# Performance work log

Measured on AMD Instinct MI355X. Metric: run time of the kernel, lower is better.

Reference implementation:

```python
import jax, jax.numpy as jnp
from jax import lax
import numpy as np

M, CLS, K, DL, DC, DO, BD = 87, 65, 128, 128, 128, 2048, 256
B, H, W = 256, 7, 7


def _c1(x, Wt, b):
    # 1x1 Conv2d: [B,Cin,H,W] -> [B,Cout,H,W]
    return jnp.einsum('oc,bchw->bohw', Wt, x) + b[None, :, None, None]


def _pagerank(edge, v_init, p=0.85, iters=100):
    # torch: transition = adj / adj.sum(dim=1)  (broadcast divides COLUMNS by row-sums)
    n = edge.shape[0]
    Wpr = p * edge / jnp.sum(edge, axis=1)[None, :]
    s = v_init * n                                  # [B,n,1]
    coef = (1.0 - p) / n
    def body(i, xv):
        zx = coef * jnp.sum(xv, axis=1, keepdims=True)      # z_T @ x -> [B,1,1]
        return jnp.einsum('ij,bjo->bio', Wpr, xv) + s * zx
    xv = lax.fori_loop(0, iters, body, s)
    nrm = jnp.sqrt(jnp.sum(xv * xv, axis=1, keepdims=True))  # F.normalize(dim=1)
    xv = xv / jnp.maximum(nrm, 1e-12)
    return (v_init + xv).reshape(v_init.shape[0], -1)        # [B,n]


def setup_inputs() -> dict:
    key = jax.random.key(0)
    ks = jax.random.split(key, 24)
    def w(k, shape, s=0.02):
        return jax.random.normal(k, shape, jnp.float32) * s
    rng = np.random.default_rng(0)
    A = (rng.random((M, M)) < 0.08).astype(np.float32)
    A = np.maximum(A, A.T)
    np.fill_diagonal(A, 1.0)   # symmetric adjacency with self-loops (degrees > 0)
    return {
        'x': jax.random.normal(ks[0], (B, DO, H, W), jnp.float32),
        'Wb': w(ks[1], (BD, DO)), 'bb': w(ks[2], (BD,), 0.01),
        'Wfc': w(ks[3], (CLS, BD)), 'Wfc2': w(ks[4], (CLS, BD)),
        'Wo1': w(ks[5], (4 * DL, DO)), 'bo1': w(ks[6], (4 * DL,), 0.01),
        'Wo2': w(ks[7], (DL, 4 * DL)), 'bo2': w(ks[8], (DL,), 0.01),
        'Wa': w(ks[9], (M, DL)), 'ba': w(ks[10], (M,), 0.01),
        'Wps': w(ks[11], (DC, DL)), 'bps': w(ks[12], (DC,), 0.01),
        'node_p': jax.random.uniform(ks[13], (K, M), jnp.float32, -0.1, 0.1),
        'Wg': w(ks[14], (DC, DC + K)), 'bg': w(ks[15], (DC,), 0.01),
        'Wsp': w(ks[16], (DL, DC)), 'bsp': w(ks[17], (DL,), 0.01),
        'Ws': w(ks[18], (1, DC + DL)), 'bs': w(ks[19], (1,), 0.01),
        'Wox1': w(ks[20], (4 * DL, DL)), 'box1': w(ks[21], (4 * DL,), 0.01),
        'Wox2': w(ks[22], (DO, 4 * DL)), 'box2': w(ks[23], (DO,), 0.01),
        'edge': jnp.asarray(A),
    }


def reference(x, Wb, bb, Wfc, Wfc2, Wo1, bo1, Wo2, bo2, Wa, ba, Wps, bps,
              node_p, Wg, bg, Wsp, bsp, Ws, bs, Wox1, box1, Wox2, box2, edge):
    Bsz, _, hl, wl = x.shape
    HW = hl * wl

    # global pooled branch
    x_p = jnp.mean(x, axis=(2, 3))                           # [B,2048]
    features_p = x_p @ Wb.T + bb                             # [B,256]
    pre_output = features_p @ Wfc.T                          # [B,65]
    pre_score = jax.nn.softmax(lax.stop_gradient(pre_output), axis=1)

    # personalized pagerank over the semantic graph (constant wrt grads)
    v_init = jnp.concatenate(
        [jnp.zeros((Bsz, M - CLS), x.dtype), pre_score], axis=1)[:, :, None]
    v_y = lax.stop_gradient(_pagerank(edge, v_init))         # [B,87]

    # local feature reduction 2048 -> 512 -> 128
    x_l = _c1(_c1(x, Wo1, bo1), Wo2, bo2)                    # [B,128,7,7]

    a = _c1(x_l, Wa, ba).reshape(Bsz, M, HW).transpose(0, 2, 1)   # [B,HW,87]
    ps = _c1(x_l, Wps, bps).reshape(Bsz, DC, HW)                  # [B,128,HW]
    m1 = jax.nn.relu(jnp.matmul(ps, a))                           # [B,128,87]

    # replicate torch's exact (k, B*m) reshape + flat v_y broadcast
    node = jnp.broadcast_to(node_p[None], (Bsz, K, M)).reshape(K, Bsz * M)
    node = (v_y.reshape(-1) * node).reshape(Bsz, K, M)

    g = jnp.einsum('oc,bcm->bom', Wg, jnp.concatenate([node, m1], axis=1)) \
        + bg[None, :, None]                                   # [B,128,87]

    # D^-1/2 A D^-1/2 graph propagation
    Dinv = jnp.sum(edge, axis=0) ** -0.5
    edge_norm = Dinv[:, None] * edge * Dinv[None, :]
    m2 = jax.nn.relu(jnp.einsum('bcm,mn->bcn', g, edge_norm))  # [B,128,87]

    sp = jnp.einsum('oc,bcm->bom', Wsp, m2) + bsp[None, :, None]  # [B,128,87]

    # conv_s over concat(m2_expand, x_expand) is separable: avoid the
    # [B,256,HW,87] tensor entirely (1 output channel, 1x1 kernel).
    Ws1, Ws2 = Ws[0, :DC], Ws[0, DC:]
    t_node = jnp.einsum('c,bcm->bm', Ws1, m2)                  # [B,87]
    t_pix = jnp.einsum('c,bcp->bp', Ws2, x_l.reshape(Bsz, DL, HW))  # [B,HW]
    s_logits = t_node[:, :, None] + t_pix[:, None, :] + bs[0]  # [B,87,HW]
    s_att = jax.nn.softmax(s_logits, axis=1)                   # softmax over nodes

    m3 = jax.nn.relu(jnp.matmul(sp, s_att)).reshape(Bsz, DL, hl, wl)
    m3 = _c1(_c1(m3, Wox1, box1), Wox2, box2)                  # [B,2048,7,7]

    feature_aug = jnp.mean(m3, axis=(2, 3)) @ Wb.T + bb
    features = features_p + feature_aug
    outputs2 = features @ Wfc2.T
    softmax_outputs = jax.nn.softmax(outputs2, axis=1)
    return (features, outputs2, softmax_outputs, pre_output, features_p)
```

## Files before the change

kernel.cpp:

```cpp
#include <hip/hip_runtime.h>
#include <cmath>


typedef __attribute__((ext_vector_type(8))) short short8;
typedef __attribute__((ext_vector_type(4))) short s16x4;
typedef __attribute__((ext_vector_type(4))) float f32x4;

constexpr size_t OFF_W12BF = 0;
constexpr size_t OFF_T1BF  = 131072;
constexpr size_t OFF_WBBF  = 262144;
constexpr size_t OFF_XPBF  = 524288;
constexpr size_t OFF_WAPBF = 786432;
constexpr size_t OFF_WG2BF = 800768;
constexpr size_t OFF_ENPBF = 808960;
constexpr size_t OFF_B215  = 813568;
constexpr size_t OFF_B12   = 813792;
constexpr size_t OFF_WPR   = 813920;
constexpr size_t OFF_BTMP  = 821496;
constexpr size_t OFF_WC    = 823544;
constexpr size_t OFF_BC    = 856312;
constexpr size_t OFF_VY    = 856568;
constexpr size_t OFF_NT    = 878848;
constexpr size_t OFF_PART  = 901376;

__device__ __forceinline__ unsigned short f2bf(float f) {
  unsigned u = __builtin_bit_cast(unsigned, f);
  u += 0x7fffu + ((u >> 16) & 1u);
  return (unsigned short)(u >> 16);
}
__device__ __forceinline__ float bf2f(unsigned short s) {
  return __builtin_bit_cast(float, ((unsigned)s) << 16);
}

__global__ __launch_bounds__(256) void ksetup_all(
    const float* __restrict__ Wb,  const float* __restrict__ bb,
    const float* __restrict__ Wa,  const float* __restrict__ ba,
    const float* __restrict__ Wps, const float* __restrict__ bps,
    const float* __restrict__ Wg,  const float* __restrict__ edge,
    const float* __restrict__ Wo2, const float* __restrict__ Wo1,
    const float* __restrict__ Wox2,const float* __restrict__ Wox1,
    const float* __restrict__ box1,const float* __restrict__ box2,
    const float* __restrict__ bo1, const float* __restrict__ bo2,
    float* __restrict__ ws, float* __restrict__ featp)
{
  __shared__ alignas(16) short As[64*72];
  __shared__ alignas(16) short Bs[64*72];
  int blk = blockIdx.x, tid = threadIdx.x;
  if (blk < 2048) {
    int idx = blk*256 + tid;
    ((unsigned short*)(ws+OFF_WBBF))[idx] = f2bf(Wb[idx]);
  } else if (blk < 2304) {
    int idx = (blk-2048)*256 + tid;
    featp[idx] = bb[idx & 255];
  } else if (blk < 2432) {
    int idx = (blk-2304)*256 + tid;
    ws[OFF_WC + idx] = 0.f;
  } else if (blk < 2544) {
    int idx = (blk-2432)*256 + tid;
    int r = idx >> 7, c = idx & 127;
    float v;
    if (r < 128)      v = Wps[r*128 + c];
    else if (r < 215) v = Wa[(r-128)*128 + c];
    else              v = 0.f;
    ((unsigned short*)(ws+OFF_WAPBF))[idx] = f2bf(v);
  } else if (blk < 2608) {
    int idx = (blk-2544)*256 + tid;
    int o = idx >> 7, d = idx & 127;
    ((unsigned short*)(ws+OFF_WG2BF))[idx] = f2bf(Wg[o*256 + 128 + d]);
  } else if (blk < 2644) {
    int idx = (blk-2608)*256 + tid;
    int m = idx / 96, n = idx % 96;
    float v = 0.f;
    if (m < 87 && n < 87) {
      float sm = 0.f, sn = 0.f;
      for (int k = 0; k < 87; ++k) { sm += edge[k*87+m]; sn += edge[k*87+n]; }
      v = edge[m*87+n] / sqrtf(sm*sn);
    }
    ((unsigned short*)(ws+OFF_ENPBF))[idx] = f2bf(v);
  } else if (blk < 2674) {
    int idx = (blk-2644)*256 + tid;
    if (idx < 87*87) {
      int j = idx % 87;
      float rs = 0.f;
      for (int k = 0; k < 87; ++k) rs += edge[j*87+k];
// ... 84 lines not shown
  const float* xb = x + ((size_t)b*2048 + q*512)*49;

  int p4A = tid % 13, cA = tid / 13;
  int tB = tid + 512;
  int p4B = tB % 13, cB = tB / 13;
  bool hasB = (tid < 320);

  float fA[4], fB[4];
  {
    if (p4A < 12) {
      float4 v = *(const float4*)(xb + cA*49 + p4A*4);
      fA[0]=v.x; fA[1]=v.y; fA[2]=v.z; fA[3]=v.w;
    } else fA[0] = xb[cA*49 + 48];
    if (hasB) {
      if (p4B < 12) {
        float4 v = *(const float4*)(xb + cB*49 + p4B*4);
        fB[0]=v.x; fB[1]=v.y; fB[2]=v.z; fB[3]=v.w;
      } else fB[0] = xb[cB*49 + 48];
    }
  }

  f32x4 acc[4];
  #pragma unroll
  for (int i = 0; i < 4; ++i) acc[i] = (f32x4)(0.f);

  for (int kci = 0; kci < 8; ++kci) {
    short* bt = Bt[kci & 1];
    if (p4A < 12) {
      #pragma unroll
      for (int i = 0; i < 4; ++i) bt[(p4A*4+i)*72 + cA] = (short)f2bf(fA[i]);
    } else bt[48*72 + cA] = (short)f2bf(fA[0]);
    if (hasB) {
      if (p4B < 12) {
        #pragma unroll
        for (int i = 0; i < 4; ++i) bt[(p4B*4+i)*72 + cB] = (short)f2bf(fB[i]);
      } else bt[48*72 + cB] = (short)f2bf(fB[0]);
    }
    __syncthreads();
    if (kci < 7) {
      const float* xc = xb + (size_t)(kci+1)*64*49;
      if (p4A < 12) {
        float4 v = *(const float4*)(xc + cA*49 + p4A*4);
        fA[0]=v.x; fA[1]=v.y; fA[2]=v.z; fA[3]=v.w;
      } else fA[0] = xc[cA*49 + 48];
      if (hasB) {
        if (p4B < 12) {
          float4 v = *(const float4*)(xc + cB*49 + p4B*4);
          fB[0]=v.x; fB[1]=v.y; fB[2]=v.z; fB[3]=v.w;
        } else fB[0] = xc[cB*49 + 48];
      }
    }
    const short* wr = w12bf + (size_t)(w*16 + lane16)*2048 + q*512 + kci*64 + quad*8;
    short8 a0 = *(const short8*)(wr);
    short8 a1 = *(const short8*)(wr + 32);
    #pragma unroll
    for (int ni = 0; ni < 4; ++ni) {
      const short* br = bt + (ni*16 + lane16)*72 + quad*8;
      short8 b0 = *(const short8*)(br);
      short8 b1 = *(const short8*)(br + 32);
      acc[ni] = __builtin_amdgcn_mfma_f32_16x16x32_bf16(a0, b0, acc[ni], 0, 0, 0);
      acc[ni] = __builtin_amdgcn_mfma_f32_16x16x32_bf16(a1, b1, acc[ni], 0, 0, 0);
    }
    if (tid < 64) {
      float s = 0.f;
      for (int p = 0; p < 49; ++p)
        s += bf2f((unsigned short)bt[p*72 + tid]);
      xpbf[(size_t)b*2048 + q*512 + kci*64 + tid] = (short)f2bf(s * (1.f/49.f));
    }
  }
  float* po = part + ((size_t)q*256 + b)*6656;
  #pragma unroll
  for (int ni = 0; ni < 4; ++ni) {
    int p = ni*16 + lane16;
    if (p < 49) {
      #pragma unroll
      for (int r = 0; r < 4; ++r) {
        int o = w*16 + quad*4 + r;
        po[o*52 + p] = acc[ni][r];
      }
    }
  }
}

__global__ __launch_bounds__(256) void kwcf(const float* __restrict__ Wb,
                                            const float* __restrict__ bb,
                                            const short* __restrict__ xpbf,
                                            float* __restrict__ featp,
                                            float* __restrict__ ws)
{
  __shared__ alignas(16) short As[64*72];
  __shared__ alignas(16) short Bs[64*72];
  int blk = blockIdx.x, tid = threadIdx.x;
  if (blk < 64) {
    const short* wbbf = (const short*)(ws+OFF_WBBF);
    const short* t1s  = (const short*)(ws+OFF_T1BF);
    int i0 = (blk & 3)*64, j0 = ((blk >> 2) & 1)*64, kc0 = (blk >> 3)*256;
    int w = tid >> 6, l = tid & 63, quad = l >> 4, lane16 = l & 15;
    f32x4 acc[4];
    #pragma unroll
    for (int i = 0; i < 4; ++i) acc[i] = (f32x4)(0.f);
    for (int kc = kc0; kc < kc0+256; kc += 64) {
      for (int t = tid; t < 512; t += 256) {
        int r = t >> 3, c8 = t & 7;
        *(short8*)&As[r*72 + c8*8] = *(const short8*)&wbbf[(size_t)(i0+r)*2048 + kc + c8*8];
      }
      for (int t = tid; t < 1024; t += 256) {
        int kr = t >> 4, n4 = t & 15;
        s16x4 v = *(const s16x4*)&t1s[(size_t)(kc+kr)*128 + j0 + n4*4];
        Bs[(n4*4+0)*72 + kr] = v[0];
        Bs[(n4*4+1)*72 + kr] = v[1];
        Bs[(n4*4+2)*72 + kr] = v[2];
        Bs[(n4*4+3)*72 + kr] = v[3];
      }
      __syncthreads();
      #pragma unroll
      for (int ks = 0; ks < 2; ++ks) {
        short8 a = *(const short8*)&As[(w*16+lane16)*72 + ks*32 + quad*8];
        #pragma unroll
        for (int nt = 0; nt < 4; ++nt) {
          short8 b8 = *(const short8*)&Bs[(nt*16+lane16)*72 + ks*32 + quad*8];
          acc[nt] = __builtin_amdgcn_mfma_f32_16x16x32_bf16(a, b8, acc[nt], 0, 0, 0);
        }
      }
      __syncthreads();
    }
    #pragma unroll
    for (int nt = 0; nt < 4; ++nt)
      #pragma unroll
      for (int r = 0; r < 4; ++r)
        atomicAdd(&ws[OFF_WC + (size_t)(i0 + w*16 + quad*4 + r)*128 + j0 + nt*16 + lane16], acc[nt][r]);
  } else if (blk < 128) {
    int j = (blk-64)*4 + (tid >> 6), l = tid & 63;
    float s = 0.f;
    for (int c = l; c < 2048; c += 64) s += Wb[(size_t)j*2048 + c] * ws[OFF_BTMP + c];
    for (int off = 32; off; off >>= 1) s += __shfl_down(s, off, 64);
    if (l == 0) ws[OFF_BC + j] = s + bb[j];
  } else {
    const short* wbbf = (const short*)(ws+OFF_WBBF);
    int idx = blk - 128;
    int i0 = (idx & 3)*64, j0 = ((idx >> 2) & 3)*64, kc0 = (idx >> 4)*256;
    int w = tid >> 6, l = tid & 63, quad = l >> 4, lane16 = l & 15;
    f32x4 acc[4];
    #pragma unroll
    for (int i = 0; i < 4; ++i) acc[i] = (f32x4)(0.f);
    for (int kc = kc0; kc < kc0+256; kc += 32) {
      short8 a = *(const short8*)&xpbf[(size_t)(i0 + w*16 + lane16)*2048 + kc + quad*8];
      #pragma unroll
      for (int nt = 0; nt < 4; ++nt) {
        short8 b8 = *(const short8*)&wbbf[(size_t)(j0 + nt*16 + lane16)*2048 + kc + quad*8];
        acc[nt] = __builtin_amdgcn_mfma_f32_16x16x32_bf16(a, b8, acc[nt], 0, 0, 0);
      }
    }
    #pragma unroll
    for (int nt = 0; nt < 4; ++nt)
      #pragma unroll
      for (int r = 0; r < 4; ++r)
        atomicAdd(&featp[(size_t)(i0 + w*16 + quad*4 + r)*256 + j0 + nt*16 + lane16], acc[nt][r]);
  }
}

__global__ __launch_bounds__(128, 1) void kpr(const float* __restrict__ featp,
                                              const float* __restrict__ Wfc,
                                              const float* __restrict__ wpr,
                                              float* __restrict__ preo,
                                              float* __restrict__ vy)
{
  __shared__ alignas(16) float fpr[256];
  __shared__ alignas(16) float po[68];
  __shared__ alignas(16) float vs[2][88];
  __shared__ float red[2];
  int b = blockIdx.x, tid = threadIdx.x;
  fpr[tid] = featp[b*256 + tid];
  fpr[tid+128] = featp[b*256 + 128 + tid];
  __syncthreads();
  if (tid < 65) {
    float s = 0.f;
    for (int c = 0; c < 256; c += 4) {
      float4 w4 = *(const float4*)&Wfc[tid*256 + c];
      s += w4.x*fpr[c] + w4.y*fpr[c+1] + w4.z*fpr[c+2] + w4.w*fpr[c+3];
    }
    po[tid] = s;
    preo[b*65 + tid] = s;
  }
  __syncthreads();
  if (tid < 64) {
    float v = po[tid];
    if (tid == 0) v = fmaxf(v, po[64]);
    float mx = v;
    #pragma unroll
    for (int off = 32; off; off >>= 1) mx = fmaxf(mx, __shfl_down(mx, off, 64));
    mx = __shfl(mx, 0, 64);
    float e = expf(po[tid]-mx) + ((tid == 0) ? expf(po[64]-mx) : 0.f);
    float sm = e;
    #pragma unroll
    for (int off = 32; off; off >>= 1) sm += __shfl_down(sm, off, 64);
    if (tid == 0) { red[0] = mx; red[1] = 1.f/sm; }
  }
  __syncthreads();
  float vinit = 0.f;
  if (tid >= 22 && tid < 87) vinit = expf(po[tid-22]-red[0]) * red[1];
  float s_i = vinit * 87.f;
  float wrow[87];
  if (tid < 87) {
    float add = s_i * (0.15f/87.0f);
    #pragma unroll
    for (int j = 0; j < 87; ++j) wrow[j] = wpr[tid*87 + j] + add;
    vs[0][tid] = s_i;
  }
  __syncthreads();
  for (int it = 0; it < 64; ++it) {
    const float* vc = vs[it & 1];
    if (tid < 87) {
      float nv = 0.f;
      #pragma unroll
      for (int j4 = 0; j4 < 21; ++j4) {
        float4 v4 = *(const float4*)&vc[j4*4];
        nv += wrow[j4*4+0]*v4.x + wrow[j4*4+1]*v4.y + wrow[j4*4+2]*v4.z + wrow[j4*4+3]*v4.w;
      }
      nv += wrow[84]*vc[84] + wrow[85]*vc[85] + wrow[86]*vc[86];
      vs[(it+1) & 1][tid] = nv;
    }
    __syncthreads();
  }
  if (tid < 64) {
    float v = vs[0][tid]*vs[0][tid];
    if (tid < 23) v += vs[0][64+tid]*vs[0][64+tid];
    #pragma unroll
    for (int off = 32; off; off >>= 1) v += __shfl_down(v, off, 64);
    if (tid == 0) red[0] = 1.f / fmaxf(sqrtf(v), 1e-12f);
  }
  __syncthreads();
  if (tid < 87) vy[b*87 + tid] = vinit + vs[0][tid]*red[0];
}

__global__ __launch_bounds__(256) void knode(const float* __restrict__ Wg,
                                             const float* __restrict__ node_p,
                                             const float* __restrict__ vy,
                                             float* __restrict__ nt)
{
  int idx = blockIdx.x*256 + threadIdx.x;
  int par = idx / 11264;
  int r = idx % 11264;
  int o = r / 88, m = r % 88;
  float v = 0.f;
  if (m < 87) {
    float s = 0.f;
    for (int k = 0; k < 128; ++k)
      s += Wg[o*256+k] * node_p[k*87+m] * vy[(par*128+k)*87+m];
    v = s;
  }
  nt[idx] = v;
}

__global__ __launch_bounds__(512) void kgraph_all(
    const float* __restrict__ part,  const float* __restrict__ b12,
    const short* __restrict__ wapbf, const float* __restrict__ b215,
    const short* __restrict__ wg2bf, const float* __restrict__ nt,
    const float* __restrict__ bg,    const short* __restrict__ enpbf,
    const float* __restrict__ Wsp,   const float* __restrict__ bsp,
    const float* __restrict__ Ws,    const float* __restrict__ wc,
    const float* __restrict__ bc,    const float* __restrict__ featp,
    const float* __restrict__ Wfc2,
    float* __restrict__ feat, float* __restrict__ out2, float* __restrict__ soft)
{
  extern __shared__ char smraw[];
  short* XT = (short*)smraw;
  short* At = XT + 8704;
  short* M1 = At + 16128;
  short* G  = M1 + 13056;
  short* M2 = G  + 13312;
  float* fb  = (float*)(M2 + 13312);
  float* wsm = fb;
  float* tnb = fb + 96;
  float* zs  = fb + 192;
  float* m3s = fb + 320;
  float* fs  = fb + 448;
  float* o2s = fb + 704;
  float* red = fb + 776;

  int b = blockIdx.x, tid = threadIdx.x;
  int w = tid >> 6, l = tid & 63, quad = l >> 4, lane16 = l & 15;

  const float* p0 = part + (size_t)b*6656;
  const float* p1 = p0 + (size_t)256*6656;
  const float* p2 = p1 + (size_t)256*6656;
  const float* p3 = p2 + (size_t)256*6656;
  for (int t = tid; t < 6656; t += 512) {
    int o = t / 52, p = t % 52;
    XT[p*136 + o] = (short)f2bf(p0[t] + p1[t] + p2[t] + p3[t] + b12[o]);
  }
  for (int t = tid; t < 1536; t += 512) {
    int p = 52 + t/128, o = t % 128;
    XT[p*136 + o] = 0;
  }
  __syncthreads();

  for (int t = w; t < 56; t += 8) {
    int mt = t >> 2, n4 = t & 3;
    f32x4 acc = (f32x4)(0.f);
    #pragma unroll
    for (int ks = 0; ks < 4; ++ks) {
      short8 a  = *(const short8*)&wapbf[(size_t)(mt*16+lane16)*128 + ks*32 + quad*8];
      short8 b8 = *(const short8*)&XT[(n4*16+lane16)*136 + ks*32 + quad*8];
      acc = __builtin_amdgcn_mfma_f32_16x16x32_bf16(a, b8, acc, 0, 0, 0);
    }
    int p = n4*16 + lane16;
    #pragma unroll
    for (int r = 0; r < 4; ++r) {
      int rr = mt*16 + quad*4 + r;
      At[rr*72 + p] = (p < 49) ? (short)f2bf(acc[r] + b215[rr]) : (short)0;
    }
  }
  __syncthreads();

  for (int t = w; t < 48; t += 8) {
    int mt = t / 8, n4 = t % 8;
    f32x4 acc = (f32x4)(0.f);
    #pragma unroll
    for (int ks = 0; ks < 2; ++ks) {
      short8 a  = *(const short8*)&At[(128 + mt*16 + lane16)*72 + ks*32 + quad*8];
      short8 b8 = *(const short8*)&At[(n4*16+lane16)*72 + ks*32 + quad*8];
      acc = __builtin_amdgcn_mfma_f32_16x16x32_bf16(a, b8, acc, 0, 0, 0);
    }
    int d = n4*16 + lane16;
    #pragma unroll
    for (int r = 0; r < 4; ++r) {
      int m = mt*16 + quad*4 + r;
      M1[m*136 + d] = (short)f2bf(fmaxf(acc[r], 0.f));
    }
  }
  __syncthreads();

  const float* ntb = nt + (size_t)(b & 1)*11264;
  for (int t = w; t < 48; t += 8) {
    int mt = t / 6, n4 = t % 6;
    f32x4 acc = (f32x4)(0.f);
    #pragma unroll
    for (int ks = 0; ks < 4; ++ks) {
      short8 a  = *(const short8*)&wg2bf[(size_t)(mt*16+lane16)*128 + ks*32 + quad*8];
      short8 b8 = *(const short8*)&M1[(n4*16+lane16)*136 + ks*32 + quad*8];
      acc = __builtin_amdgcn_mfma_f32_16x16x32_bf16(a, b8, acc, 0, 0, 0);
    }
    int m = n4*16 + lane16;
    #pragma unroll
    for (int r = 0; r < 4; ++r) {
      int o = mt*16 + quad*4 + r;
      float v = acc[r] + bg[o] + ((m < 88) ? ntb[o*88 + m] : 0.f);
      G[o*104 + m] = (short)f2bf(v);
    }
  }
  __syncthreads();

  for (int t = w; t < 48; t += 8) {
    int mt = t / 6, n4 = t % 6;
    f32x4 acc = (f32x4)(0.f);
    #pragma unroll
    for (int ks = 0; ks < 3; ++ks) {
      short8 a  = *(const short8*)&G[(mt*16+lane16)*104 + ks*32 + quad*8];
      short8 b8 = *(const short8*)&enpbf[(size_t)(n4*16+lane16)*96 + ks*32 + quad*8];
      acc = __builtin_amdgcn_mfma_f32_16x16x32_bf16(a, b8, acc, 0, 0, 0);
    }
    int n = n4*16 + lane16;
    #pragma unroll
    for (int r = 0; r < 4; ++r) {
      int c = mt*16 + quad*4 + r;
      M2[c*104 + n] = (short)f2bf(fmaxf(acc[r], 0.f));
    }
  }
  __syncthreads();

  if (tid < 87) {
    float s = 0.f;
    for (int c = 0; c < 128; ++c) s += Ws[c] * bf2f((unsigned short)M2[c*104 + tid]);
    tnb[tid] = s;
  }
  __syncthreads();
  if (tid < 64) {
    float v = tnb[tid];
    if (tid < 23) v = fmaxf(v, tnb[64+tid]);
    float mx = v;
    #pragma unroll
    for (int off = 32; off; off >>= 1) mx = fmaxf(mx, __shfl_down(mx, off, 64));
    mx = __shfl(mx, 0, 64);
    float e0 = expf(tnb[tid]-mx);
    float e1 = (tid < 23) ? expf(tnb[64+tid]-mx) : 0.f;
    float sm = e0 + e1;
    #pragma unroll
    for (int off = 32; off; off >>= 1) sm += __shfl_down(sm, off, 64);
    sm = __shfl(sm, 0, 64);
    float inv = 1.f/sm;
    wsm[tid] = e0*inv;
    if (tid < 23) wsm[64+tid] = e1*inv;
  }
  __syncthreads();
  if (tid < 128) {
    float s = 0.f;
    for (int m = 0; m < 87; ++m) s += bf2f((unsigned short)M2[tid*104 + m]) * wsm[m];
    zs[tid] = s;
  }
  __syncthreads();
  if (tid < 128) {
    float s = 0.f;
    for (int c = 0; c < 128; ++c) s += Wsp[tid*128 + c] * zs[c];
    m3s[tid] = fmaxf(s + bsp[tid], 0.f);
  }
  __syncthreads();

  if (tid < 256) {
    float s = 0.f;
    #pragma unroll 4
    for (int d4 = 0; d4 < 32; ++d4) {
      float4 w4 = *(const float4*)&wc[tid*128 + d4*4];
      s += w4.x*m3s[d4*4] + w4.y*m3s[d4*4+1] + w4.z*m3s[d4*4+2] + w4.w*m3s[d4*4+3];
    }
    float f = featp[b*256 + tid] + bc[tid] + s;
    fs[tid] = f;
    feat[b*256 + tid] = f;
  }
  __syncthreads();
  if (tid < 65) {
    float s = 0.f;
    for (int j = 0; j < 256; ++j) s += Wfc2[tid*256 + j] * fs[j];
    out2[b*65 + tid] = s;
    o2s[tid] = s;
  }
  __syncthreads();
  if (tid < 64) {
    float v = o2s[tid];
    if (tid == 0) v = fmaxf(v, o2s[64]);
    float mx = v;
    #pragma unroll
    for (int off = 32; off; off >>= 1) mx = fmaxf(mx, __shfl_down(mx, off, 64));
    mx = __shfl(mx, 0, 64);
    float e = expf(o2s[tid]-mx) + ((tid == 0) ? expf(o2s[64]-mx) : 0.f);
    float sm = e;
    #pragma unroll
    for (int off = 32; off; off >>= 1) sm += __shfl_down(sm, off, 64);
    if (tid == 0) { red[0] = mx; red[1] = 1.f/sm; }
  }
  __syncthreads();
  if (tid < 65) soft[b*65 + tid] = expf(o2s[tid]-red[0]) * red[1];
}

extern "C" void kernel_launch(void* const* d_in, const int* in_sizes, int n_in,
                              void* d_out, int out_size, void* d_ws, size_t ws_size,
                              hipStream_t stream)
{
  (void)in_sizes; (void)n_in; (void)out_size; (void)ws_size;
  const float* x      = (const float*)d_in[0];
  const float* Wb     = (const float*)d_in[1];
  const float* bb     = (const float*)d_in[2];
  const float* Wfc    = (const float*)d_in[3];
  const float* Wfc2   = (const float*)d_in[4];
  const float* Wo1    = (const float*)d_in[5];
  const float* bo1    = (const float*)d_in[6];
  const float* Wo2    = (const float*)d_in[7];
  const float* bo2    = (const float*)d_in[8];
  const float* Wa     = (const float*)d_in[9];
  const float* ba     = (const float*)d_in[10];
  const float* Wps    = (const float*)d_in[11];
  const float* bps    = (const float*)d_in[12];
  const float* node_p = (const float*)d_in[13];
  const float* Wg     = (const float*)d_in[14];
  const float* bg     = (const float*)d_in[15];
  const float* Wsp    = (const float*)d_in[16];
  const float* bsp    = (const float*)d_in[17];
  const float* Ws     = (const float*)d_in[18];
  const float* Wox1   = (const float*)d_in[20];
  const float* box1   = (const float*)d_in[21];
  const float* Wox2   = (const float*)d_in[22];
  const float* box2   = (const float*)d_in[23];
  const float* edge   = (const float*)d_in[24];

  float* ws   = (float*)d_ws;
  float* out  = (float*)d_out;
  float* feat  = out;
  float* out2  = out + 65536;
  float* soft  = out + 82176;
  float* preo  = out + 98816;
  float* featp = out + 115456;

  ksetup_all<<<3347, 256, 0, stream>>>(Wb, bb, Wa, ba, Wps, bps, Wg, edge,
                                       Wo2, Wo1, Wox2, Wox1, box1, box2, bo1, bo2,
                                       ws, featp);
  kmain5<<<dim3(256,4), 512, 0, stream>>>(x, (const short*)(ws + OFF_W12BF),
                                          (short*)(ws + OFF_XPBF), ws + OFF_PART);
  kwcf<<<256, 256, 0, stream>>>(Wb, bb, (const short*)(ws + OFF_XPBF), featp, ws);
  kpr<<<256, 128, 0, stream>>>(featp, Wfc, ws + OFF_WPR, preo, ws + OFF_VY);
  knode<<<88, 256, 0, stream>>>(Wg, node_p, ws + OFF_VY, ws + OFF_NT);
  kgraph_all<<<256, 512, 132144, stream>>>(ws + OFF_PART, ws + OFF_B12,
                                           (const short*)(ws + OFF_WAPBF),
                                           ws + OFF_B215,
                                           (const short*)(ws + OFF_WG2BF),
                                           ws + OFF_NT, bg,
                                           (const short*)(ws + OFF_ENPBF),
                                           Wsp, bsp, Ws,
                                           ws + OFF_WC, ws + OFF_BC, featp, Wfc2,
                                           feat, out2, soft);
}
```

Before: 363.0 us.

## Merge tail kernels into one cooperative kernel with grid syncs

Replaces the four tail launches (kwcf, kpr, knode, kgraph_all) with a single cooperative kernel of 256 blocks x 512 threads that separates the phases with grid.sync(). The goal is to cut launch and inter-kernel gap overhead. Several small per-block loops (Wfc GEMV, the PageRank matvec, the node contraction, the Ws/Wsp/Wfc2 reductions) now split work four ways across lanes and combine with shuffles. The cost is that a 132 KB LDS allocation limits occupancy to one block per CU, so all 256 blocks must be co-resident, and the grid barriers add their own latency.

```diff
diff --git a/kernel.cpp b/kernel.cpp
--- a/kernel.cpp
+++ b/kernel.cpp
@@ -1,5 +1,8 @@
 #include <hip/hip_runtime.h>
+#include <hip/hip_cooperative_groups.h>
 #include <cmath>
+
+namespace cg = cooperative_groups;
 
 
 typedef __attribute__((ext_vector_type(8))) short short8;
@@ -250,364 +253,402 @@
   }
 }
 
-__global__ __launch_bounds__(256) void kwcf(const float* __restrict__ Wb,
-                                            const float* __restrict__ bb,
-                                            const short* __restrict__ xpbf,
-                                            float* __restrict__ featp,
-                                            float* __restrict__ ws)
-{
-  __shared__ alignas(16) short As[64*72];
-  __shared__ alignas(16) short Bs[64*72];
-  int blk = blockIdx.x, tid = threadIdx.x;
-  if (blk < 64) {
-    const short* wbbf = (const short*)(ws+OFF_WBBF);
-    const short* t1s  = (const short*)(ws+OFF_T1BF);
-    int i0 = (blk & 3)*64, j0 = ((blk >> 2) & 1)*64, kc0 = (blk >> 3)*256;
-    int w = tid >> 6, l = tid & 63, quad = l >> 4, lane16 = l & 15;
-    f32x4 acc[4];
-    #pragma unroll
-    for (int i = 0; i < 4; ++i) acc[i] = (f32x4)(0.f);
-    for (int kc = kc0; kc < kc0+256; kc += 64) {
-      for (int t = tid; t < 512; t += 256) {
-        int r = t >> 3, c8 = t & 7;
-        *(short8*)&As[r*72 + c8*8] = *(const short8*)&wbbf[(size_t)(i0+r)*2048 + kc + c8*8];
-      }
-      for (int t = tid; t < 1024; t += 256) {
-        int kr = t >> 4, n4 = t & 15;
-        s16x4 v = *(const s16x4*)&t1s[(size_t)(kc+kr)*128 + j0 + n4*4];
-        Bs[(n4*4+0)*72 + kr] = v[0];
-        Bs[(n4*4+1)*72 + kr] = v[1];
-        Bs[(n4*4+2)*72 + kr] = v[2];
-        Bs[(n4*4+3)*72 + kr] = v[3];
-      }
-      __syncthreads();
-      #pragma unroll
-      for (int ks = 0; ks < 2; ++ks) {
-        short8 a = *(const short8*)&As[(w*16+lane16)*72 + ks*32 + quad*8];
-        #pragma unroll
-        for (int nt = 0; nt < 4; ++nt) {
-          short8 b8 = *(const short8*)&Bs[(nt*16+lane16)*72 + ks*32 + quad*8];
-          acc[nt] = __builtin_amdgcn_mfma_f32_16x16x32_bf16(a, b8, acc[nt], 0, 0, 0);
-        }
-      }
-      __syncthreads();
-    }
-    #pragma unroll
-    for (int nt = 0; nt < 4; ++nt)
-      #pragma unroll
-      for (int r = 0; r < 4; ++r)
-        atomicAdd(&ws[OFF_WC + (size_t)(i0 + w*16 + quad*4 + r)*128 + j0 + nt*16 + lane16], acc[nt][r]);
-  } else if (blk < 128) {
-    int j = (blk-64)*4 + (tid >> 6), l = tid & 63;
-    float s = 0.f;
-    for (int c = l; c < 2048; c += 64) s += Wb[(size_t)j*2048 + c] * ws[OFF_BTMP + c];
-    for (int off = 32; off; off >>= 1) s += __shfl_down(s, off, 64);
-    if (l == 0) ws[OFF_BC + j] = s + bb[j];
-  } else {
-    const short* wbbf = (const short*)(ws+OFF_WBBF);
-    int idx = blk - 128;
-    int i0 = (idx & 3)*64, j0 = ((idx >> 2) & 3)*64, kc0 = (idx >> 4)*256;
-    int w = tid >> 6, l = tid & 63, quad = l >> 4, lane16 = l & 15;
-    f32x4 acc[4];
-    #pragma unroll
-    for (int i = 0; i < 4; ++i) acc[i] = (f32x4)(0.f);
-    for (int kc = kc0; kc < kc0+256; kc += 32) {
-      short8 a = *(const short8*)&xpbf[(size_t)(i0 + w*16 + lane16)*2048 + kc + quad*8];
-      #pragma unroll
-      for (int nt = 0; nt < 4; ++nt) {
-        short8 b8 = *(const short8*)&wbbf[(size_t)(j0 + nt*16 + lane16)*2048 + kc + quad*8];
-        acc[nt] = __builtin_amdgcn_mfma_f32_16x16x32_bf16(a, b8, acc[nt], 0, 0, 0);
-      }
-    }
-    #pragma unroll
-    for (int nt = 0; nt < 4; ++nt)
-      #pragma unroll
-      for (int r = 0; r < 4; ++r)
-        atomicAdd(&featp[(size_t)(i0 + w*16 + quad*4 + r)*256 + j0 + nt*16 + lane16], acc[nt][r]);
-  }
-}
-
-__global__ __launch_bounds__(128, 1) void kpr(const float* __restrict__ featp,
-                                              const float* __restrict__ Wfc,
-                                              const float* __restrict__ wpr,
-                                              float* __restrict__ preo,
-                                              float* __restrict__ vy)
-{
-  __shared__ alignas(16) float fpr[256];
-  __shared__ alignas(16) float po[68];
-  __shared__ alignas(16) float vs[2][88];
-  __shared__ float red[2];
-  int b = blockIdx.x, tid = threadIdx.x;
-  fpr[tid] = featp[b*256 + tid];
-  fpr[tid+128] = featp[b*256 + 128 + tid];
-  __syncthreads();
-  if (tid < 65) {
-    float s = 0.f;
-    for (int c = 0; c < 256; c += 4) {
-      float4 w4 = *(const float4*)&Wfc[tid*256 + c];
-      s += w4.x*fpr[c] + w4.y*fpr[c+1] + w4.z*fpr[c+2] + w4.w*fpr[c+3];
-    }
-    po[tid] = s;
-    preo[b*65 + tid] = s;
-  }
-  __syncthreads();
-  if (tid < 64) {
-    float v = po[tid];
-    if (tid == 0) v = fmaxf(v, po[64]);
-    float mx = v;
-    #pragma unroll
-    for (int off = 32; off; off >>= 1) mx = fmaxf(mx, __shfl_down(mx, off, 64));
-    mx = __shfl(mx, 0, 64);
-    float e = expf(po[tid]-mx) + ((tid == 0) ? expf(po[64]-mx) : 0.f);
-    float sm = e;
-    #pragma unroll
-    for (int off = 32; off; off >>= 1) sm += __shfl_down(sm, off, 64);
-    if (tid == 0) { red[0] = mx; red[1] = 1.f/sm; }
-  }
-  __syncthreads();
-  float vinit = 0.f;
-  if (tid >= 22 && tid < 87) vinit = expf(po[tid-22]-red[0]) * red[1];
-  float s_i = vinit * 87.f;
-  float wrow[87];
-  if (tid < 87) {
-    float add = s_i * (0.15f/87.0f);
-    #pragma unroll
-    for (int j = 0; j < 87; ++j) wrow[j] = wpr[tid*87 + j] + add;
-    vs[0][tid] = s_i;
-  }
-  __syncthreads();
-  for (int it = 0; it < 64; ++it) {
-    const float* vc = vs[it & 1];
-    if (tid < 87) {
-      float nv = 0.f;
-      #pragma unroll
-      for (int j4 = 0; j4 < 21; ++j4) {
-        float4 v4 = *(const float4*)&vc[j4*4];
-        nv += wrow[j4*4+0]*v4.x + wrow[j4*4+1]*v4.y + wrow[j4*4+2]*v4.z + wrow[j4*4+3]*v4.w;
-      }
-      nv += wrow[84]*vc[84] + wrow[85]*vc[85] + wrow[86]*vc[86];
-      vs[(it+1) & 1][tid] = nv;
-    }
-    __syncthreads();
-  }
-  if (tid < 64) {
-    float v = vs[0][tid]*vs[0][tid];
-    if (tid < 23) v += vs[0][64+tid]*vs[0][64+tid];
-    #pragma unroll
-    for (int off = 32; off; off >>= 1) v += __shfl_down(v, off, 64);
-    if (tid == 0) red[0] = 1.f / fmaxf(sqrtf(v), 1e-12f);
-  }
-  __syncthreads();
-  if (tid < 87) vy[b*87 + tid] = vinit + vs[0][tid]*red[0];
-}
-
-__global__ __launch_bounds__(256) void knode(const float* __restrict__ Wg,
-                                             const float* __restrict__ node_p,
-                                             const float* __restrict__ vy,
-                                             float* __restrict__ nt)
-{
-  int idx = blockIdx.x*256 + threadIdx.x;
-  int par = idx / 11264;
-  int r = idx % 11264;
-  int o = r / 88, m = r % 88;
-  float v = 0.f;
-  if (m < 87) {
-    float s = 0.f;
-    for (int k = 0; k < 128; ++k)
-      s += Wg[o*256+k] * node_p[k*87+m] * vy[(par*128+k)*87+m];
-    v = s;
-  }
-  nt[idx] = v;
-}
-
-__global__ __launch_bounds__(512) void kgraph_all(
-    const float* __restrict__ part,  const float* __restrict__ b12,
-    const short* __restrict__ wapbf, const float* __restrict__ b215,
-    const short* __restrict__ wg2bf, const float* __restrict__ nt,
-    const float* __restrict__ bg,    const short* __restrict__ enpbf,
-    const float* __restrict__ Wsp,   const float* __restrict__ bsp,
-    const float* __restrict__ Ws,    const float* __restrict__ wc,
-    const float* __restrict__ bc,    const float* __restrict__ featp,
-    const float* __restrict__ Wfc2,
-    float* __restrict__ feat, float* __restrict__ out2, float* __restrict__ soft)
+__global__ __launch_bounds__(512) void ktail(
+    const float* __restrict__ Wb,  const float* __restrict__ bb,
+    const float* __restrict__ Wfc, const float* __restrict__ Wg,
+    const float* __restrict__ node_p, const float* __restrict__ bg,
+    const float* __restrict__ Wsp, const float* __restrict__ bsp,
+    const float* __restrict__ Ws,  const float* __restrict__ Wfc2,
+    const short* __restrict__ xpbf,
+    float* __restrict__ ws, float* __restrict__ featp,
+    float* __restrict__ preo, float* __restrict__ feat,
+    float* __restrict__ out2, float* __restrict__ soft)
 {
   extern __shared__ char smraw[];
-  short* XT = (short*)smraw;
-  short* At = XT + 8704;
-  short* M1 = At + 16128;
-  short* G  = M1 + 13056;
-  short* M2 = G  + 13312;
-  float* fb  = (float*)(M2 + 13312);
-  float* wsm = fb;
-  float* tnb = fb + 96;
-  float* zs  = fb + 192;
-  float* m3s = fb + 320;
-  float* fs  = fb + 448;
-  float* o2s = fb + 704;
-  float* red = fb + 776;
-
-  int b = blockIdx.x, tid = threadIdx.x;
-  int w = tid >> 6, l = tid & 63, quad = l >> 4, lane16 = l & 15;
-
-  const float* p0 = part + (size_t)b*6656;
-  const float* p1 = p0 + (size_t)256*6656;
-  const float* p2 = p1 + (size_t)256*6656;
-  const float* p3 = p2 + (size_t)256*6656;
-  for (int t = tid; t < 6656; t += 512) {
-    int o = t / 52, p = t % 52;
-    XT[p*136 + o] = (short)f2bf(p0[t] + p1[t] + p2[t] + p3[t] + b12[o]);
+  cg::grid_group grid = cg::this_grid();
+  const int tid = threadIdx.x;
+  const int bx = blockIdx.x;
+
+  {
+    int sub = tid >> 8, stid = tid & 255;
+    int oblk = bx*2 + sub;
+    if (bx < 128) {
+      if (oblk < 64) {
+        short* As = (short*)(smraw + sub*18432);
+        short* Bs = As + 4608;
+        const short* wbbf = (const short*)(ws+OFF_WBBF);
+        const short* t1s  = (const short*)(ws+OFF_T1BF);
+        int i0 = (oblk & 3)*64, j0 = ((oblk >> 2) & 1)*64, kc0 = (oblk >> 3)*256;
+        int w = stid >> 6, l = stid & 63, quad = l >> 4, lane16 = l & 15;
+        f32x4 acc[4];
+        #pragma unroll
+        for (int i = 0; i < 4; ++i) acc[i] = (f32x4)(0.f);
+        for (int kc = kc0; kc < kc0+256; kc += 64) {
+          for (int t = stid; t < 512; t += 256) {
+            int r = t >> 3, c8 = t & 7;
+            *(short8*)&As[r*72 + c8*8] = *(const short8*)&wbbf[(size_t)(i0+r)*2048 + kc + c8*8];
+          }
+          for (int t = stid; t < 1024; t += 256) {
+            int kr = t >> 4, n4 = t & 15;
+            s16x4 v = *(const s16x4*)&t1s[(size_t)(kc+kr)*128 + j0 + n4*4];
+            Bs[(n4*4+0)*72 + kr] = v[0];
+            Bs[(n4*4+1)*72 + kr] = v[1];
+            Bs[(n4*4+2)*72 + kr] = v[2];
+            Bs[(n4*4+3)*72 + kr] = v[3];
+          }
+          __syncthreads();
+          #pragma unroll
+          for (int ks = 0; ks < 2; ++ks) {
+            short8 a = *(const short8*)&As[(w*16+lane16)*72 + ks*32 + quad*8];
+            #pragma unroll
+            for (int nt4 = 0; nt4 < 4; ++nt4) {
+              short8 b8 = *(const short8*)&Bs[(nt4*16+lane16)*72 + ks*32 + quad*8];
+              acc[nt4] = __builtin_amdgcn_mfma_f32_16x16x32_bf16(a, b8, acc[nt4], 0, 0, 0);
+            }
+          }
+          __syncthreads();
+        }
+        #pragma unroll
+        for (int nt4 = 0; nt4 < 4; ++nt4)
+          #pragma unroll
+          for (int r = 0; r < 4; ++r)
+            atomicAdd(&ws[OFF_WC + (size_t)(i0 + w*16 + quad*4 + r)*128 + j0 + nt4*16 + lane16], acc[nt4][r]);
+      } else if (oblk < 128) {
+        int j = (oblk-64)*4 + (stid >> 6), l = stid & 63;
+        float s = 0.f;
+        for (int c = l; c < 2048; c += 64) s += Wb[(size_t)j*2048 + c] * ws[OFF_BTMP + c];
+        for (int off = 32; off; off >>= 1) s += __shfl_down(s, off, 64);
+        if (l == 0) ws[OFF_BC + j] = s + bb[j];
+      } else {
+        const short* wbbf = (const short*)(ws+OFF_WBBF);
+        int idx = oblk - 128;
+        int i0 = (idx & 3)*64, j0 = ((idx >> 2) & 3)*64, kc0 = (idx >> 4)*256;
+        int w = stid >> 6, l = stid & 63, quad = l >> 4, lane16 = l & 15;
+        f32x4 acc[4];
+        #pragma unroll
+        for (int i = 0; i < 4; ++i) acc[i] = (f32x4)(0.f);
+        for (int kc = kc0; kc < kc0+256; kc += 32) {
+          short8 a = *(const short8*)&xpbf[(size_t)(i0 + w*16 + lane16)*2048 + kc + quad*8];
+          #pragma unroll
+          for (int nt4 = 0; nt4 < 4; ++nt4) {
+            short8 b8 = *(const short8*)&wbbf[(size_t)(j0 + nt4*16 + lane16)*2048 + kc + quad*8];
+            acc[nt4] = __builtin_amdgcn_mfma_f32_16x16x32_bf16(a, b8, acc[nt4], 0, 0, 0);
+          }
+        }
+        #pragma unroll
+        for (int nt4 = 0; nt4 < 4; ++nt4)
+          #pragma unroll
+          for (int r = 0; r < 4; ++r)
+            atomicAdd(&featp[(size_t)(i0 + w*16 + quad*4 + r)*256 + j0 + nt4*16 + lane16], acc[nt4][r]);
+      }
+    }
   }
-  for (int t = tid; t < 1536; t += 512) {
-    int p = 52 + t/128, o = t % 128;
-    XT[p*136 + o] = 0;
+  grid.sync();
+
+  {
+    float* fb2 = (float*)smraw;
+    float* fpr = fb2;
+    float* po  = fb2 + 256;
+    float* vsA = fb2 + 324;
+    float* vsB = fb2 + 412;
+    float* vis = fb2 + 500;
+    float* rd  = fb2 + 588;
+    const float* __restrict__ wpr = ws + OFF_WPR;
+    const int b = bx;
+    if (tid < 256) fpr[tid] = featp[b*256 + tid];
+    __syncthreads();
+    if (tid < 260) {
+      int row = tid >> 2, p = tid & 3;
+      float s = 0.f;
+      const float* wr = Wfc + row*256 + p*64;
+      #pragma unroll
+      for (int c = 0; c < 64; c += 4) {
+        float4 w4 = *(const float4*)&wr[c];
+        s += w4.x*fpr[p*64+c] + w4.y*fpr[p*64+c+1] + w4.z*fpr[p*64+c+2] + w4.w*fpr[p*64+c+3];
+      }
+      s += __shfl_xor(s, 1, 64);
+      s += __shfl_xor(s, 2, 64);
+      if (p == 0) { po[row] = s; preo[b*65 + row] = s; }
+    }
+    __syncthreads();
+    if (tid < 64) {
+      float v = po[tid];
+      if (tid == 0) v = fmaxf(v, po[64]);
+      float mx = v;
+      #pragma unroll
+      for (int off = 32; off; off >>= 1) mx = fmaxf(mx, __shfl_down(mx, off, 64));
+      mx = __shfl(mx, 0, 64);
+      float e = expf(po[tid]-mx) + ((tid == 0) ? expf(po[64]-mx) : 0.f);
+      float sm = e;
+      #pragma unroll
+      for (int off = 32; off; off >>= 1) sm += __shfl_down(sm, off, 64);
+      if (tid == 0) { rd[0] = mx; rd[1] = 1.f/sm; }
+    }
+    __syncthreads();
+    if (tid < 88) {
+      float vin = (tid >= 22 && tid < 87) ? expf(po[tid-22]-rd[0])*rd[1] : 0.f;
+      vis[tid] = vin;
+      vsA[tid] = vin * 87.f;
+      vsB[tid] = 0.f;
+    }
+    __syncthreads();
+    float wrow[22];
+    const int m4 = tid >> 2, pp = tid & 3;
+    if (tid < 348) {
+      float add = vis[m4] * 0.15f;
+      #pragma unroll
+      for (int jj = 0; jj < 22; ++jj) {
+        int j = pp*22 + jj;
+        wrow[jj] = (j < 87) ? (wpr[m4*87 + j] + add) : 0.f;
+      }
+    }
+    for (int it = 0; it < 64; ++it) {
+      const float* vc = (it & 1) ? vsB : vsA;
+      float* vn = (it & 1) ? vsA : vsB;
+      if (tid < 348) {
+        float nv = 0.f;
+        #pragma unroll
+        for (int jj = 0; jj < 22; ++jj) nv += wrow[jj] * vc[pp*22 + jj];
+        nv += __shfl_xor(nv, 1, 64);
+        nv += __shfl_xor(nv, 2, 64);
+        if (pp == 0) vn[m4] = nv;
+      }
+      __syncthreads();
+    }
+    if (tid < 64) {
+      float v = vsA[tid]*vsA[tid];
+      if (tid < 23) v += vsA[64+tid]*vsA[64+tid];
+      #pragma unroll
+      for (int off = 32; off; off >>= 1) v += __shfl_down(v, off, 64);
+      if (tid == 0) rd[2] = 1.f / fmaxf(sqrtf(v), 1e-12f);
+    }
+    __syncthreads();
+    if (tid < 87) ws[OFF_VY + b*87 + tid] = vis[tid] + vsA[tid]*rd[2];
   }
-  __syncthreads();
-
-  for (int t = w; t < 56; t += 8) {
-    int mt = t >> 2, n4 = t & 3;
-    f32x4 acc = (f32x4)(0.f);
-    #pragma unroll
-    for (int ks = 0; ks < 4; ++ks) {
-      short8 a  = *(const short8*)&wapbf[(size_t)(mt*16+lane16)*128 + ks*32 + quad*8];
-      short8 b8 = *(const short8*)&XT[(n4*16+lane16)*136 + ks*32 + quad*8];
-      acc = __builtin_amdgcn_mfma_f32_16x16x32_bf16(a, b8, acc, 0, 0, 0);
-    }
-    int p = n4*16 + lane16;
-    #pragma unroll
-    for (int r = 0; r < 4; ++r) {
-      int rr = mt*16 + quad*4 + r;
-      At[rr*72 + p] = (p < 49) ? (short)f2bf(acc[r] + b215[rr]) : (short)0;
-    }
+  grid.sync();
+
+  if (tid < 352) {
+    const float* __restrict__ vyp = ws + OFF_VY;
+    int out = bx*88 + (tid >> 2);
+    int par = out / 11264;
+    int r = out % 11264;
+    int o = r / 88, m = r % 88;
+    int p = tid & 3;
+    float s = 0.f;
+    if (m < 87) {
+      const float* vrow = vyp + (size_t)(par*128)*87 + m;
+      for (int k = p*32; k < p*32+32; ++k)
+        s += Wg[o*256 + k] * node_p[k*87 + m] * vrow[k*87];
+    }
+    s += __shfl_xor(s, 1, 64);
+    s += __shfl_xor(s, 2, 64);
+    if (p == 0) ws[OFF_NT + out] = s;
   }
-  __syncthreads();
-
-  for (int t = w; t < 48; t += 8) {
-    int mt = t / 8, n4 = t % 8;
-    f32x4 acc = (f32x4)(0.f);
-    #pragma unroll
-    for (int ks = 0; ks < 2; ++ks) {
-      short8 a  = *(const short8*)&At[(128 + mt*16 + lane16)*72 + ks*32 + quad*8];
-      short8 b8 = *(const short8*)&At[(n4*16+lane16)*72 + ks*32 + quad*8];
-      acc = __builtin_amdgcn_mfma_f32_16x16x32_bf16(a, b8, acc, 0, 0, 0);
-    }
-    int d = n4*16 + lane16;
-    #pragma unroll
-    for (int r = 0; r < 4; ++r) {
-      int m = mt*16 + quad*4 + r;
-      M1[m*136 + d] = (short)f2bf(fmaxf(acc[r], 0.f));
-    }
+  grid.sync();
+
+  {
+    short* XT = (short*)smraw;
+    short* At = XT + 8704;
+    short* M1 = At + 16128;
+    short* G  = M1 + 13056;
+    short* M2 = G  + 13312;
+    float* fb  = (float*)(M2 + 13312);
+    float* wsm = fb;
+    float* tnb = fb + 96;
+    float* zs  = fb + 192;
+    float* m3s = fb + 320;
+    float* fs  = fb + 448;
+    float* o2s = fb + 704;
+    float* red = fb + 776;
+
+    const int b = bx;
+    int w = tid >> 6, l = tid & 63, quad = l >> 4, lane16 = l & 15;
+
+    const float* __restrict__ part  = ws + OFF_PART;
+    const float* __restrict__ b12   = ws + OFF_B12;
+    const short* __restrict__ wapbf = (const short*)(ws + OFF_WAPBF);
+    const float* __restrict__ b215  = ws + OFF_B215;
+    const short* __restrict__ wg2bf = (const short*)(ws + OFF_WG2BF);
+    const short* __restrict__ enpbf = (const short*)(ws + OFF_ENPBF);
+    const float* __restrict__ wc    = ws + OFF_WC;
+    const float* __restrict__ bc    = ws + OFF_BC;
+    const float* __restrict__ ntb   = ws + OFF_NT + (size_t)(b & 1)*11264;
+
+    const float* p0 = part + (size_t)b*6656;
+    const float* p1 = p0 + (size_t)256*6656;
+    const float* p2 = p1 + (size_t)256*6656;
+    const float* p3 = p2 + (size_t)256*6656;
+    for (int t = tid; t < 6656; t += 512) {
+      int o = t / 52, p = t % 52;
+      XT[p*136 + o] = (short)f2bf(p0[t] + p1[t] + p2[t] + p3[t] + b12[o]);
+    }
+    for (int t = tid; t < 1536; t += 512) {
+      int p = 52 + t/128, o = t % 128;
+      XT[p*136 + o] = 0;
+    }
+    __syncthreads();
+
+    for (int t = w; t < 56; t += 8) {
+      int mt = t >> 2, n4 = t & 3;
+      f32x4 acc = (f32x4)(0.f);
+      #pragma unroll
+      for (int ks = 0; ks < 4; ++ks) {
+        short8 a  = *(const short8*)&wapbf[(size_t)(mt*16+lane16)*128 + ks*32 + quad*8];
+        short8 b8 = *(const short8*)&XT[(n4*16+lane16)*136 + ks*32 + quad*8];
+        acc = __builtin_amdgcn_mfma_f32_16x16x32_bf16(a, b8, acc, 0, 0, 0);
+      }
+      int p = n4*16 + lane16;
+      #pragma unroll
+      for (int r = 0; r < 4; ++r) {
+        int rr = mt*16 + quad*4 + r;
+        At[rr*72 + p] = (p < 49) ? (short)f2bf(acc[r] + b215[rr]) : (short)0;
+      }
+    }
+    __syncthreads();
+
+    for (int t = w; t < 48; t += 8) {
+      int mt = t / 8, n4 = t % 8;
+      f32x4 acc = (f32x4)(0.f);
+      #pragma unroll
+      for (int ks = 0; ks < 2; ++ks) {
+        short8 a  = *(const short8*)&At[(128 + mt*16 + lane16)*72 + ks*32 + quad*8];
+        short8 b8 = *(const short8*)&At[(n4*16+lane16)*72 + ks*32 + quad*8];
+        acc = __builtin_amdgcn_mfma_f32_16x16x32_bf16(a, b8, acc, 0, 0, 0);
+      }
+      int d = n4*16 + lane16;
+      #pragma unroll
+      for (int r = 0; r < 4; ++r) {
+        int m = mt*16 + quad*4 + r;
+        M1[m*136 + d] = (short)f2bf(fmaxf(acc[r], 0.f));
+      }
+    }
+    __syncthreads();
+
+    for (int t = w; t < 48; t += 8) {
+      int mt = t / 6, n4 = t % 6;
+      f32x4 acc = (f32x4)(0.f);
+      #pragma unroll
+      for (int ks = 0; ks < 4; ++ks) {
+        short8 a  = *(const short8*)&wg2bf[(size_t)(mt*16+lane16)*128 + ks*32 + quad*8];
+        short8 b8 = *(const short8*)&M1[(n4*16+lane16)*136 + ks*32 + quad*8];
+        acc = __builtin_amdgcn_mfma_f32_16x16x32_bf16(a, b8, acc, 0, 0, 0);
+      }
+      int m = n4*16 + lane16;
+      #pragma unroll
+      for (int r = 0; r < 4; ++r) {
+        int o = mt*16 + quad*4 + r;
+        float v = acc[r] + bg[o] + ((m < 88) ? ntb[o*88 + m] : 0.f);
+        G[o*104 + m] = (short)f2bf(v);
+      }
+    }
+    __syncthreads();
+
+    for (int t = w; t < 48; t += 8) {
+      int mt = t / 6, n4 = t % 6;
+      f32x4 acc = (f32x4)(0.f);
+      #pragma unroll
+      for (int ks = 0; ks < 3; ++ks) {
+        short8 a  = *(const short8*)&G[(mt*16+lane16)*104 + ks*32 + quad*8];
+        short8 b8 = *(const short8*)&enpbf[(size_t)(n4*16+lane16)*96 + ks*32 + quad*8];
+        acc = __builtin_amdgcn_mfma_f32_16x16x32_bf16(a, b8, acc, 0, 0, 0);
+      }
+      int n = n4*16 + lane16;
+      #pragma unroll
+      for (int r = 0; r < 4; ++r) {
+        int c = mt*16 + quad*4 + r;
+        M2[c*104 + n] = (short)f2bf(fmaxf(acc[r], 0.f));
+      }
+    }
+    __syncthreads();
+
+    if (tid < 348) {
+      int m = tid >> 2, p = tid & 3;
+      float s = 0.f;
+      for (int c = p*32; c < p*32+32; ++c)
+        s += Ws[c] * bf2f((unsigned short)M2[c*104 + m]);
+      s += __shfl_xor(s, 1, 64);
+      s += __shfl_xor(s, 2, 64);
+      if (p == 0) tnb[m] = s;
+    }
+    __syncthreads();
+    if (tid < 64) {
+      float v = tnb[tid];
+      if (tid < 23) v = fmaxf(v, tnb[64+tid]);
+      float mx = v;
+      #pragma unroll
+      for (int off = 32; off; off >>= 1) mx = fmaxf(mx, __shfl_down(mx, off, 64));
+      mx = __shfl(mx, 0, 64);
+      float e0 = expf(tnb[tid]-mx);
+      float e1 = (tid < 23) ? expf(tnb[64+tid]-mx) : 0.f;
+      float sm = e0 + e1;
+      #pragma unroll
+      for (int off = 32; off; off >>= 1) sm += __shfl_down(sm, off, 64);
+      sm = __shfl(sm, 0, 64);
+      float inv = 1.f/sm;
+      wsm[tid] = e0*inv;
+      if (tid < 23) wsm[64+tid] = e1*inv;
+    }
+    __syncthreads();
+    {
+      int c = tid >> 2, p = tid & 3;
+      float s = 0.f;
+      for (int mm = p*22; mm < p*22+22 && mm < 87; ++mm)
+        s += bf2f((unsigned short)M2[c*104 + mm]) * wsm[mm];
+      s += __shfl_xor(s, 1, 64);
+      s += __shfl_xor(s, 2, 64);
+      if (p == 0) zs[c] = s;
+    }
+    __syncthreads();
+    {
+      int d = tid >> 2, p = tid & 3;
+      float s = 0.f;
+      for (int c = p*32; c < p*32+32; ++c) s += Wsp[d*128 + c] * zs[c];
+      s += __shfl_xor(s, 1, 64);
+      s += __shfl_xor(s, 2, 64);
+      if (p == 0) m3s[d] = fmaxf(s + bsp[d], 0.f);
+    }
+    __syncthreads();
+
+    if (tid < 256) {
+      float s = 0.f;
+      #pragma unroll 4
+      for (int d4 = 0; d4 < 32; ++d4) {
+        float4 w4 = *(const float4*)&wc[tid*128 + d4*4];
+        s += w4.x*m3s[d4*4] + w4.y*m3s[d4*4+1] + w4.z*m3s[d4*4+2] + w4.w*m3s[d4*4+3];
+      }
+      float f = featp[b*256 + tid] + bc[tid] + s;
+      fs[tid] = f;
+      feat[b*256 + tid] = f;
+    }
+    __syncthreads();
+    if (tid < 260) {
+      int row = tid >> 2, p = tid & 3;
+      float s = 0.f;
+      for (int c = p*64; c < p*64+64; c += 4) {
+        float4 w4 = *(const float4*)&Wfc2[row*256 + c];
+        s += w4.x*fs[c] + w4.y*fs[c+1] + w4.z*fs[c+2] + w4.w*fs[c+3];
+      }
+      s += __shfl_xor(s, 1, 64);
+      s += __shfl_xor(s, 2, 64);
+      if (p == 0) { out2[b*65 + row] = s; o2s[row] = s; }
+    }
+    __syncthreads();
+    if (tid < 64) {
+      float v = o2s[tid];
+      if (tid == 0) v = fmaxf(v, o2s[64]);
+      float mx = v;
+      #pragma unroll
+      for (int off = 32; off; off >>= 1) mx = fmaxf(mx, __shfl_down(mx, off, 64));
+      mx = __shfl(mx, 0, 64);
+      float e = expf(o2s[tid]-mx) + ((tid == 0) ? expf(o2s[64]-mx) : 0.f);
+      float sm = e;
+      #pragma unroll
+      for (int off = 32; off; off >>= 1) sm += __shfl_down(sm, off, 64);
+      if (tid == 0) { red[0] = mx; red[1] = 1.f/sm; }
+    }
+    __syncthreads();
+    if (tid < 65) soft[b*65 + tid] = expf(o2s[tid]-red[0]) * red[1];
   }
-  __syncthreads();
-
-  const float* ntb = nt + (size_t)(b & 1)*11264;
-  for (int t = w; t < 48; t += 8) {
-    int mt = t / 6, n4 = t % 6;
-    f32x4 acc = (f32x4)(0.f);
-    #pragma unroll
-    for (int ks = 0; ks < 4; ++ks) {
-      short8 a  = *(const short8*)&wg2bf[(size_t)(mt*16+lane16)*128 + ks*32 + quad*8];
-      short8 b8 = *(const short8*)&M1[(n4*16+lane16)*136 + ks*32 + quad*8];
-      acc = __builtin_amdgcn_mfma_f32_16x16x32_bf16(a, b8, acc, 0, 0, 0);
-    }
-    int m = n4*16 + lane16;
-    #pragma unroll
-    for (int r = 0; r < 4; ++r) {
-      int o = mt*16 + quad*4 + r;
-      float v = acc[r] + bg[o] + ((m < 88) ? ntb[o*88 + m] : 0.f);
-      G[o*104 + m] = (short)f2bf(v);
-    }
-  }
-  __syncthreads();
-
-  for (int t = w; t < 48; t += 8) {
-    int mt = t / 6, n4 = t % 6;
-    f32x4 acc = (f32x4)(0.f);
-    #pragma unroll
-    for (int ks = 0; ks < 3; ++ks) {
-      short8 a  = *(const short8*)&G[(mt*16+lane16)*104 + ks*32 + quad*8];
-      short8 b8 = *(const short8*)&enpbf[(size_t)(n4*16+lane16)*96 + ks*32 + quad*8];
-      acc = __builtin_amdgcn_mfma_f32_16x16x32_bf16(a, b8, acc, 0, 0, 0);
-    }
-    int n = n4*16 + lane16;
-    #pragma unroll
-    for (int r = 0; r < 4; ++r) {
-      int c = mt*16 + quad*4 + r;
-      M2[c*104 + n] = (short)f2bf(fmaxf(acc[r], 0.f));
-    }
-  }
-  __syncthreads();
-
-  if (tid < 87) {
-    float s = 0.f;
-    for (int c = 0; c < 128; ++c) s += Ws[c] * bf2f((unsigned short)M2[c*104 + tid]);
-    tnb[tid] = s;
-  }
-  __syncthreads();
-  if (tid < 64) {
-    float v = tnb[tid];
-    if (tid < 23) v = fmaxf(v, tnb[64+tid]);
-    float mx = v;
-    #pragma unroll
-    for (int off = 32; off; off >>= 1) mx = fmaxf(mx, __shfl_down(mx, off, 64));
-    mx = __shfl(mx, 0, 64);
-    float e0 = expf(tnb[tid]-mx);
-    float e1 = (tid < 23) ? expf(tnb[64+tid]-mx) : 0.f;
-    float sm = e0 + e1;
-    #pragma unroll
-    for (int off = 32; off; off >>= 1) sm += __shfl_down(sm, off, 64);
-    sm = __shfl(sm, 0, 64);
-    float inv = 1.f/sm;
-    wsm[tid] = e0*inv;
-    if (tid < 23) wsm[64+tid] = e1*inv;
-  }
-  __syncthreads();
-  if (tid < 128) {
-    float s = 0.f;
-    for (int m = 0; m < 87; ++m) s += bf2f((unsigned short)M2[tid*104 + m]) * wsm[m];
-    zs[tid] = s;
-  }
-  __syncthreads();
-  if (tid < 128) {
-    float s = 0.f;
-    for (int c = 0; c < 128; ++c) s += Wsp[tid*128 + c] * zs[c];
-    m3s[tid] = fmaxf(s + bsp[tid], 0.f);
-  }
-  __syncthreads();
-
-  if (tid < 256) {
-    float s = 0.f;
-    #pragma unroll 4
-    for (int d4 = 0; d4 < 32; ++d4) {
-      float4 w4 = *(const float4*)&wc[tid*128 + d4*4];
-      s += w4.x*m3s[d4*4] + w4.y*m3s[d4*4+1] + w4.z*m3s[d4*4+2] + w4.w*m3s[d4*4+3];
-    }
-    float f = featp[b*256 + tid] + bc[tid] + s;
-    fs[tid] = f;
-    feat[b*256 + tid] = f;
-  }
-  __syncthreads();
-  if (tid < 65) {
-    float s = 0.f;
-    for (int j = 0; j < 256; ++j) s += Wfc2[tid*256 + j] * fs[j];
-    out2[b*65 + tid] = s;
-    o2s[tid] = s;
-  }
-  __syncthreads();
-  if (tid < 64) {
-    float v = o2s[tid];
-    if (tid == 0) v = fmaxf(v, o2s[64]);
-    float mx = v;
-    #pragma unroll
-    for (int off = 32; off; off >>= 1) mx = fmaxf(mx, __shfl_down(mx, off, 64));
-    mx = __shfl(mx, 0, 64);
-    float e = expf(o2s[tid]-mx) + ((tid == 0) ? expf(o2s[64]-mx) : 0.f);
-    float sm = e;
-    #pragma unroll
-    for (int off = 32; off; off >>= 1) sm += __shfl_down(sm, off, 64);
-    if (tid == 0) { red[0] = mx; red[1] = 1.f/sm; }
-  }
-  __syncthreads();
-  if (tid < 65) soft[b*65 + tid] = expf(o2s[tid]-red[0]) * red[1];
 }
 
 extern "C" void kernel_launch(void* const* d_in, const int* in_sizes, int n_in,
@@ -653,16 +694,11 @@
                                        ws, featp);
   kmain5<<<dim3(256,4), 512, 0, stream>>>(x, (const short*)(ws + OFF_W12BF),
                                           (short*)(ws + OFF_XPBF), ws + OFF_PART);
-  kwcf<<<256, 256, 0, stream>>>(Wb, bb, (const short*)(ws + OFF_XPBF), featp, ws);
-  kpr<<<256, 128, 0, stream>>>(featp, Wfc, ws + OFF_WPR, preo, ws + OFF_VY);
-  knode<<<88, 256, 0, stream>>>(Wg, node_p, ws + OFF_VY, ws + OFF_NT);
-  kgraph_all<<<256, 512, 132144, stream>>>(ws + OFF_PART, ws + OFF_B12,
-                                           (const short*)(ws + OFF_WAPBF),
-                                           ws + OFF_B215,
-                                           (const short*)(ws + OFF_WG2BF),
-                                           ws + OFF_NT, bg,
-                                           (const short*)(ws + OFF_ENPBF),
-                                           Wsp, bsp, Ws,
-                                           ws + OFF_WC, ws + OFF_BC, featp, Wfc2,
-                                           feat, out2, soft);
+  const short* xpbf_p = (const short*)(ws + OFF_XPBF);
+  void* ta[17] = {
+    (void*)&Wb, (void*)&bb, (void*)&Wfc, (void*)&Wg, (void*)&node_p, (void*)&bg,
+    (void*)&Wsp, (void*)&bsp, (void*)&Ws, (void*)&Wfc2, (void*)&xpbf_p,
+    (void*)&ws, (void*)&featp, (void*)&preo, (void*)&feat, (void*)&out2, (void*)&soft
+  };
+  hipLaunchCooperativeKernel((const void*)ktail, dim3(256), dim3(512), ta, 132144u, stream);
 }
```

After: 453.2 us. 1.25x slower.
